# Kernel tuning notes

Hardware: AMD Instinct MI355X
Metric: run time of the kernel (lower is better)

The kernel has to match this reference:

```python
import jax, jax.numpy as jnp
import numpy as np

B, S, F, H = 256, 512, 64, 128
ODE_STEPS = 4
MAX_DT = 1.0


def setup_inputs() -> dict:
    key = jax.random.key(0)
    ks = jax.random.split(key, 11)
    D = F + H  # concat(x_t, h) width
    xav = float(np.sqrt(6.0 / (D + H)))          # xavier_uniform for gate weights
    bsc = float(1.0 / np.sqrt(D))                # torch Linear default bias init
    x = jax.random.normal(ks[0], (B, S, F), jnp.float32)
    time_diffs = jax.random.uniform(ks[1], (B, S), jnp.float32, 0.1, 2.0)
    def w(k):
        return jax.random.uniform(k, (D, H), jnp.float32, -xav, xav)
    def b(k):
        return jax.random.uniform(k, (H,), jnp.float32, -bsc, bsc)
    return {
        "x": x, "time_diffs": time_diffs,
        "W_i": w(ks[2]), "b_i": b(ks[3]),
        "W_f": w(ks[4]), "b_f": b(ks[5]),
        "W_o": w(ks[6]), "b_o": b(ks[7]),
        "W_g": w(ks[8]), "b_g": b(ks[9]),
    }


def reference(x, time_diffs, W_i, b_i, W_f, b_f, W_o, b_o, W_g, b_g):
    def ode_func(x_t, h, c):
        comb = jnp.concatenate([x_t, h], axis=-1)  # [B, F+H]
        i = jax.nn.sigmoid(comb @ W_i + b_i)
        f = jax.nn.sigmoid(comb @ W_f + b_f)
        o = jax.nn.sigmoid(comb @ W_o + b_o)
        g = jnp.tanh(comb @ W_g + b_g)
        dc = i * g + f * c - c
        dh = o * jnp.tanh(c) - h
        return dh, dc

    def rk4_step(x_t, h, c, dt):  # dt: [B, 1]
        k1h, k1c = ode_func(x_t, h, c)
        k2h, k2c = ode_func(x_t, h + 0.5 * dt * k1h, c + 0.5 * dt * k1c)
        k3h, k3c = ode_func(x_t, h + 0.5 * dt * k2h, c + 0.5 * dt * k2c)
        k4h, k4c = ode_func(x_t, h + dt * k3h, c + dt * k3c)
        h_new = h + dt / 6.0 * (k1h + 2 * k2h + 2 * k3h + k4h)
        c_new = c + dt / 6.0 * (k1c + 2 * k2c + 2 * k3c + k4c)
        return h_new, c_new

    def time_step(carry, inp):
        h, c = carry
        x_t, dtv = inp  # x_t [B,F], dtv [B]
        sub_dt = (jnp.minimum(dtv, MAX_DT) / ODE_STEPS)[:, None]  # [B,1]
        def body(hc, _):
            hh, cc = hc
            return rk4_step(x_t, hh, cc, sub_dt), None
        (h, c), _ = jax.lax.scan(body, (h, c), None, length=ODE_STEPS)
        return (h, c), h

    h0 = jnp.zeros((x.shape[0], H), x.dtype)
    c0 = jnp.zeros((x.shape[0], H), x.dtype)
    xs = (jnp.swapaxes(x, 0, 1), jnp.swapaxes(time_diffs, 0, 1))  # [S,B,F], [S,B]
    _, hs = jax.lax.scan(time_step, (h0, c0), xs)  # [S,B,H]
    return jnp.swapaxes(hs, 0, 1)  # [B,S,H]
```

## Files before the change

kernel.cpp:

```cpp
#include <hip/hip_runtime.h>


#define B_N 256
#define S_N 512
#define F_N 64
#define H_N 128

typedef _Float16 v8h __attribute__((ext_vector_type(8)));
typedef float v4f __attribute__((ext_vector_type(4)));

#define PIN_V(x) asm("" : "+v"(x))
#define MFMA16(a, b, c) __builtin_amdgcn_mfma_f32_16x16x32_f16((a), (b), (c), 0, 0, 0)
#define SB0() __builtin_amdgcn_sched_barrier(0)
#define BAR() do { SB0(); \
                   asm volatile("s_waitcnt lgkmcnt(0)" ::: "memory"); \
                   __builtin_amdgcn_s_barrier(); SB0(); } while (0)

static __device__ __forceinline__ float sigm(float x) {
  float e = __builtin_amdgcn_exp2f(-1.442695040888963f * x);
  return __builtin_amdgcn_rcpf(1.0f + e);
}

__global__ void __launch_bounds__(512, 2) clstm_mfma10(
    const float* __restrict__ x,
    const float* __restrict__ td,
    const float* __restrict__ Wi, const float* __restrict__ bi,
    const float* __restrict__ Wf, const float* __restrict__ bff,
    const float* __restrict__ Wo, const float* __restrict__ bo,
    const float* __restrict__ Wg, const float* __restrict__ bg,
    float* __restrict__ out)
{
  const int b    = blockIdx.x;
  const int t    = threadIdx.x;
  const int wv   = t >> 6;
  const int l    = t & 63;
  const int col  = l & 15;
  const int quad = l >> 4;
  const int n    = wv * 16 + col;

  const float* Wptr[4] = {Wi, Wf, Wo, Wg};

  v8h Bh[4][4];
  v8h Bx[4][2];
#pragma unroll
  for (int g = 0; g < 4; ++g) {
    const float* W = Wptr[g];
#pragma unroll
    for (int kt = 0; kt < 4; ++kt) {
      v8h f;
#pragma unroll
      for (int j = 0; j < 8; ++j)
        f[j] = (_Float16)W[(64 + kt * 32 + quad * 8 + j) * H_N + n];
      Bh[g][kt] = f;
      PIN_V(Bh[g][kt]);
    }
#pragma unroll
    for (int kt = 0; kt < 2; ++kt) {
      v8h f;
#pragma unroll
      for (int j = 0; j < 8; ++j)
        f[j] = (_Float16)W[(kt * 32 + quad * 8 + j) * H_N + n];
      Bx[g][kt] = f;
      PIN_V(Bx[g][kt]);
    }
  }
  float bias[4];
#pragma unroll
  for (int g = 0; g < 4; ++g)
    bias[g] = (g == 0 ? bi : g == 1 ? bff : g == 2 ? bo : bg)[n];

  __shared__ alignas(16) _Float16 lds_h[2][H_N];
  __shared__ alignas(16) _Float16 lds_x[F_N];
  __shared__ float lds_td[S_N];

  lds_td[t] = td[b * S_N + t];
  if (t < 32) {
    const float* xr = x + (size_t)b * S_N * F_N;
    lds_x[2 * t]     = (_Float16)xr[2 * t];
    lds_x[2 * t + 1] = (_Float16)xr[2 * t + 1];
  }
  if (t < H_N) lds_h[0][t] = (_Float16)0.0f;

  float h0v = 0.f, c0v = 0.f;
  float h_ev = 0.f, c_ev = 0.f;
  float sum_h = 0.f, sum_c = 0.f;
  float dt = 0.f, hdt = 0.f, d6 = 0.f, d6p = 0.f;
  const v4f zf = {0.f, 0.f, 0.f, 0.f};
  v4f ci2 = zf, ci3 = zf, cf2 = zf, cf3 = zf, cg2 = zf, cg3 = zf;
  v4f xpI = zf, xpF = zf, xpO = zf, xpG = zf;
  float xn0 = 0.f, xn1 = 0.f;

  for (int s = 0; s < S_N; ++s) {
#pragma unroll
    for (int ode = 0; ode < 4; ++ode) {
#pragma unroll
      for (int st = 0; st < 4; ++st) {
        BAR();
        const _Float16* hb = lds_h[st & 1];
        v8h ah0 = *(const v8h*)(hb + quad * 8);
        v8h ah1 = *(const v8h*)(hb + 32 + quad * 8);
        v8h ah2 = *(const v8h*)(hb + 64 + quad * 8);
        v8h ah3 = *(const v8h*)(hb + 96 + quad * 8);

        if (ode == 0 && st == 0) {
          dt  = fminf(lds_td[s], 1.0f) * 0.25f;
          hdt = 0.5f * dt;
          d6  = dt * (1.0f / 6.0f);
          v8h ax0 = *(const v8h*)(lds_x + quad * 8);
          v8h ax1 = *(const v8h*)(lds_x + 32 + quad * 8);
          {
            v4f cb = {bias[0], bias[0], bias[0], bias[0]};
            v4f a = MFMA16(ax0, Bx[0][0], cb);  xpI = MFMA16(ax1, Bx[0][1], a);
          }
          {
            v4f cb = {bias[1], bias[1], bias[1], bias[1]};
            v4f a = MFMA16(ax0, Bx[1][0], cb);  xpF = MFMA16(ax1, Bx[1][1], a);
          }
          {
            v4f cb = {bias[2], bias[2], bias[2], bias[2]};
            v4f a = MFMA16(ax0, Bx[2][0], cb);  xpO = MFMA16(ax1, Bx[2][1], a);
          }
          {
            v4f cb = {bias[3], bias[3], bias[3], bias[3]};
            v4f a = MFMA16(ax0, Bx[3][0], cb);  xpG = MFMA16(ax1, Bx[3][1], a);
          }
          xn0 = 0.f; xn1 = 0.f;
          if (t < 32 && s + 1 < S_N) {
            const float* xr = x + (size_t)(b * S_N + s + 1) * F_N;
            xn0 = xr[2 * t]; xn1 = xr[2 * t + 1];
          }
        }

        v4f co0 = MFMA16(ah0, Bh[2][0], xpO);
        v4f co1 = MFMA16(ah1, Bh[2][1], zf);
        v4f co2 = MFMA16(ah2, Bh[2][2], zf);
        v4f co3 = MFMA16(ah3, Bh[2][3], zf);
        SB0();

        float tc;
        {
          const int pr = (st == 0) ? 3 : st - 1;
          float pi = ci2[0] + ci3[0];
          float pf = cf2[0] + cf3[0];
          float pg = cg2[0] + cg3[0];
          float ai = sigm(pi);
          float af = sigm(pf);
          float ag = fmaf(2.0f, sigm(2.0f * pg), -1.0f);
          float kc = fmaf(ai, ag, (af - 1.0f) * c_ev);
          float cnx;
          if (pr == 0)      { sum_c = kc;                      cnx = fmaf(hdt, kc, c0v); }
          else if (pr == 1) { sum_c = fmaf(2.f, kc, sum_c);    cnx = fmaf(hdt, kc, c0v); }
          else if (pr == 2) { sum_c = fmaf(2.f, kc, sum_c);    cnx = fmaf(dt, kc, c0v); }
          else {
            float sc = sum_c + kc;
            float dd = (ode == 0 && st == 0) ? d6p : d6;
            c0v = fmaf(dd, sc, c0v);
            cnx = c0v;
          }
          c_ev = cnx;
          tc = fmaf(2.0f, sigm(2.0f * c_ev), -1.0f);
        }

        float po = (co0[0] + co1[0]) + (co2[0] + co3[0]);
        float ao = sigm(po);
        float kh = fmaf(ao, tc, -h_ev);
        float hnx;
        if (st == 0)      { sum_h = kh;                      hnx = fmaf(hdt, kh, h0v); }
        else if (st == 1) { sum_h = fmaf(2.f, kh, sum_h);    hnx = fmaf(hdt, kh, h0v); }
        else if (st == 2) { sum_h = fmaf(2.f, kh, sum_h);    hnx = fmaf(dt, kh, h0v); }
        else {
          float sh = sum_h + kh;
          h0v = fmaf(d6, sh, h0v);
          hnx = h0v;
        }
        h_ev = hnx;
        if (quad == 0) lds_h[(st & 1) ^ 1][n] = (_Float16)hnx;
        SB0();

        ci2 = MFMA16(ah0, Bh[0][0], xpI);
        ci2 = MFMA16(ah1, Bh[0][1], ci2);
        ci3 = MFMA16(ah2, Bh[0][2], zf);
        ci3 = MFMA16(ah3, Bh[0][3], ci3);
        cf2 = MFMA16(ah0, Bh[1][0], xpF);
        cf2 = MFMA16(ah1, Bh[1][1], cf2);
        cf3 = MFMA16(ah2, Bh[1][2], zf);
        cf3 = MFMA16(ah3, Bh[1][3], cf3);
        cg2 = MFMA16(ah0, Bh[3][0], xpG);
        cg2 = MFMA16(ah1, Bh[3][1], cg2);
        cg3 = MFMA16(ah2, Bh[3][2], zf);
        cg3 = MFMA16(ah3, Bh[3][3], cg3);
        SB0();

        if (ode == 3 && st == 3) {
          if (t < 32 && s + 1 < S_N) {
            lds_x[2 * t]     = (_Float16)xn0;
            lds_x[2 * t + 1] = (_Float16)xn1;
          }
          if (quad == 0) out[(size_t)(b * S_N + s) * H_N + n] = h0v;
          d6p = d6;
        }
      }
    }
  }
}

extern "C" void kernel_launch(void* const* d_in, const int* in_sizes, int n_in,
                              void* d_out, int out_size, void* d_ws, size_t ws_size,
                              hipStream_t stream) {
  (void)in_sizes; (void)n_in; (void)d_ws; (void)ws_size; (void)out_size;
  clstm_mfma10<<<B_N, 512, 0, stream>>>(
      (const float*)d_in[0],
      (const float*)d_in[1],
      (const float*)d_in[2], (const float*)d_in[3],
      (const float*)d_in[4], (const float*)d_in[5],
      (const float*)d_in[6], (const float*)d_in[7],
      (const float*)d_in[8], (const float*)d_in[9],
      (float*)d_out);
}
```

Measured before the change: 3.406 ms.

## Stagger IFG MFMA and gate-activation order across wave parities

Splits waves into two parity groups. One group runs the i/f/g-gate activation math before issuing the i/f/g MFMA block, the other issues the MFMAs first. The IFG MFMAs now come before the h update and LDS store instead of after. The goal is for waves sharing a SIMD to interleave matrix-core work with transcendental VALU work, so the two units overlap rather than contend. This adds divergent code paths by wave, plus register pinning that could raise register pressure.

Measured after the change: 3.952 ms. 1.16x slower.

```diff
diff --git a/kernel.cpp b/kernel.cpp
--- a/kernel.cpp
+++ b/kernel.cpp
@@ -16,12 +16,40 @@
                    asm volatile("s_waitcnt lgkmcnt(0)" ::: "memory"); \
                    __builtin_amdgcn_s_barrier(); SB0(); } while (0)
 
+#define IFG_BLOCK() do { \
+  ci2 = MFMA16(ah0, Bh[0][0], xpI); ci2 = MFMA16(ah1, Bh[0][1], ci2); \
+  ci3 = MFMA16(ah2, Bh[0][2], zf);  ci3 = MFMA16(ah3, Bh[0][3], ci3); \
+  cf2 = MFMA16(ah0, Bh[1][0], xpF); cf2 = MFMA16(ah1, Bh[1][1], cf2); \
+  cf3 = MFMA16(ah2, Bh[1][2], zf);  cf3 = MFMA16(ah3, Bh[1][3], cf3); \
+  cg2 = MFMA16(ah0, Bh[3][0], xpG); cg2 = MFMA16(ah1, Bh[3][1], cg2); \
+  cg3 = MFMA16(ah2, Bh[3][2], zf);  cg3 = MFMA16(ah3, Bh[3][3], cg3); \
+} while (0)
+
+#define S1_BLOCK(PR, CROSS) do { \
+  float ai = sigm(pi); \
+  float af = sigm(pf); \
+  float ag = fmaf(2.0f, sigm(2.0f * pg), -1.0f); \
+  float kc = fmaf(ai, ag, (af - 1.0f) * c_ev); \
+  float cnx; \
+  if ((PR) == 0)      { sum_c = kc;                   cnx = fmaf(hdt, kc, c0v); } \
+  else if ((PR) == 1) { sum_c = fmaf(2.f, kc, sum_c); cnx = fmaf(hdt, kc, c0v); } \
+  else if ((PR) == 2) { sum_c = fmaf(2.f, kc, sum_c); cnx = fmaf(dt, kc, c0v); } \
+  else { \
+    float sc = sum_c + kc; \
+    float dd = (CROSS) ? d6p : d6; \
+    c0v = fmaf(dd, sc, c0v); \
+    cnx = c0v; \
+  } \
+  c_ev = cnx; \
+  tc = fmaf(2.0f, sigm(2.0f * c_ev), -1.0f); \
+} while (0)
+
 static __device__ __forceinline__ float sigm(float x) {
   float e = __builtin_amdgcn_exp2f(-1.442695040888963f * x);
   return __builtin_amdgcn_rcpf(1.0f + e);
 }
 
-__global__ void __launch_bounds__(512, 2) clstm_mfma10(
+__global__ void __launch_bounds__(512, 2) clstm_mfma11(
     const float* __restrict__ x,
     const float* __restrict__ td,
     const float* __restrict__ Wi, const float* __restrict__ bi,
@@ -37,6 +65,7 @@
   const int col  = l & 15;
   const int quad = l >> 4;
   const int n    = wv * 16 + col;
+  const int par  = (wv ^ (wv >> 2)) & 1;
 
   const float* Wptr[4] = {Wi, Wf, Wo, Wg};
 
@@ -135,31 +164,29 @@
         v4f co1 = MFMA16(ah1, Bh[2][1], zf);
         v4f co2 = MFMA16(ah2, Bh[2][2], zf);
         v4f co3 = MFMA16(ah3, Bh[2][3], zf);
+
+        float pi = ci2[0] + ci3[0];
+        float pf = cf2[0] + cf3[0];
+        float pg = cg2[0] + cg3[0];
+        const int pr = (st == 0) ? 3 : st - 1;
+        const bool cross = (ode == 0 && st == 0);
+        float tc;
         SB0();
 
-        float tc;
-        {
-          const int pr = (st == 0) ? 3 : st - 1;
-          float pi = ci2[0] + ci3[0];
-          float pf = cf2[0] + cf3[0];
-          float pg = cg2[0] + cg3[0];
-          float ai = sigm(pi);
-          float af = sigm(pf);
-          float ag = fmaf(2.0f, sigm(2.0f * pg), -1.0f);
-          float kc = fmaf(ai, ag, (af - 1.0f) * c_ev);
-          float cnx;
-          if (pr == 0)      { sum_c = kc;                      cnx = fmaf(hdt, kc, c0v); }
-          else if (pr == 1) { sum_c = fmaf(2.f, kc, sum_c);    cnx = fmaf(hdt, kc, c0v); }
-          else if (pr == 2) { sum_c = fmaf(2.f, kc, sum_c);    cnx = fmaf(dt, kc, c0v); }
-          else {
-            float sc = sum_c + kc;
-            float dd = (ode == 0 && st == 0) ? d6p : d6;
-            c0v = fmaf(dd, sc, c0v);
-            cnx = c0v;
-          }
-          c_ev = cnx;
-          tc = fmaf(2.0f, sigm(2.0f * c_ev), -1.0f);
-        }
+        if (par) {
+          PIN_V(pi); PIN_V(pf); PIN_V(pg);
+          S1_BLOCK(pr, cross);
+          SB0();
+          PIN_V(ah0); PIN_V(ah1); PIN_V(ah2); PIN_V(ah3);
+          IFG_BLOCK();
+        } else {
+          PIN_V(ah0); PIN_V(ah1); PIN_V(ah2); PIN_V(ah3);
+          IFG_BLOCK();
+          SB0();
+          PIN_V(pi); PIN_V(pf); PIN_V(pg);
+          S1_BLOCK(pr, cross);
+        }
+        SB0();
 
         float po = (co0[0] + co1[0]) + (co2[0] + co3[0]);
         float ao = sigm(po);
@@ -175,21 +202,6 @@
         }
         h_ev = hnx;
         if (quad == 0) lds_h[(st & 1) ^ 1][n] = (_Float16)hnx;
-        SB0();
-
-        ci2 = MFMA16(ah0, Bh[0][0], xpI);
-        ci2 = MFMA16(ah1, Bh[0][1], ci2);
-        ci3 = MFMA16(ah2, Bh[0][2], zf);
-        ci3 = MFMA16(ah3, Bh[0][3], ci3);
-        cf2 = MFMA16(ah0, Bh[1][0], xpF);
-        cf2 = MFMA16(ah1, Bh[1][1], cf2);
-        cf3 = MFMA16(ah2, Bh[1][2], zf);
-        cf3 = MFMA16(ah3, Bh[1][3], cf3);
-        cg2 = MFMA16(ah0, Bh[3][0], xpG);
-        cg2 = MFMA16(ah1, Bh[3][1], cg2);
-        cg3 = MFMA16(ah2, Bh[3][2], zf);
-        cg3 = MFMA16(ah3, Bh[3][3], cg3);
-        SB0();
 
         if (ode == 3 && st == 3) {
           if (t < 32 && s + 1 < S_N) {
@@ -208,7 +220,7 @@
                               void* d_out, int out_size, void* d_ws, size_t ws_size,
                               hipStream_t stream) {
   (void)in_sizes; (void)n_in; (void)d_ws; (void)ws_size; (void)out_size;
-  clstm_mfma10<<<B_N, 512, 0, stream>>>(
+  clstm_mfma11<<<B_N, 512, 0, stream>>>(
       (const float*)d_in[0],
       (const float*)d_in[1],
       (const float*)d_in[2], (const float*)d_in[3],
```

## Specialize waves into gate-preactivation producers and output/state-update consumers via LDS

Applied to the files above, without the earlier changes.

Splits the eight waves into two roles. Four waves compute the i/f/g gate preactivations for 32 columns each and publish them to a double-buffered LDS array. The other four compute the o-gate, read the i/f/g values one stage later and perform the cell and hidden state updates. This replaces uniform per-wave work, where each wave ran all four gates and the full update serially, with a split that overlaps the gate MFMAs and the update math across waves. In exchange it adds LDS traffic and more registers per wave, since each wave now holds weights for two column tiles, and it leaves the two roles with unequal work.

Measured after the change: 4.773 ms. +40.1%, slower.

```diff
diff --git a/kernel.cpp b/kernel.cpp
--- a/kernel.cpp
+++ b/kernel.cpp
@@ -9,7 +9,6 @@
 typedef _Float16 v8h __attribute__((ext_vector_type(8)));
 typedef float v4f __attribute__((ext_vector_type(4)));
 
-#define PIN_V(x) asm("" : "+v"(x))
 #define MFMA16(a, b, c) __builtin_amdgcn_mfma_f32_16x16x32_f16((a), (b), (c), 0, 0, 0)
 #define SB0() __builtin_amdgcn_sched_barrier(0)
 #define BAR() do { SB0(); \
@@ -21,7 +20,37 @@
   return __builtin_amdgcn_rcpf(1.0f + e);
 }
 
-__global__ void __launch_bounds__(512, 2) clstm_mfma10(
+#define UPD(SUF) do { \
+  float ai = sigm(pi_##SUF); \
+  float af = sigm(pf_##SUF); \
+  float ag = fmaf(2.0f, sigm(2.0f * pg_##SUF), -1.0f);        \
+  float kc = fmaf(ai, ag, (af - 1.0f) * c_ev_##SUF);          \
+  float cnx; \
+  if (pr == 0)      { sum_c_##SUF = kc;                         cnx = fmaf(hdt, kc, c0v_##SUF); } \
+  else if (pr == 1) { sum_c_##SUF = fmaf(2.f, kc, sum_c_##SUF); cnx = fmaf(hdt, kc, c0v_##SUF); } \
+  else if (pr == 2) { sum_c_##SUF = fmaf(2.f, kc, sum_c_##SUF); cnx = fmaf(dt, kc, c0v_##SUF); } \
+  else { \
+    float sc = sum_c_##SUF + kc; \
+    float dd = cross ? d6p : d6;                               \
+    c0v_##SUF = fmaf(dd, sc, c0v_##SUF); \
+    cnx = c0v_##SUF; \
+  } \
+  c_ev_##SUF = cnx; \
+  float tc = fmaf(2.0f, sigm(2.0f * c_ev_##SUF), -1.0f);      \
+  float ao = sigm(co_##SUF[0]); \
+  float kh = fmaf(ao, tc, -h_ev_##SUF);                       \
+  if (st == 0)      { sum_h_##SUF = kh;                         hnx_##SUF = fmaf(hdt, kh, h0v_##SUF); } \
+  else if (st == 1) { sum_h_##SUF = fmaf(2.f, kh, sum_h_##SUF); hnx_##SUF = fmaf(hdt, kh, h0v_##SUF); } \
+  else if (st == 2) { sum_h_##SUF = fmaf(2.f, kh, sum_h_##SUF); hnx_##SUF = fmaf(dt, kh, h0v_##SUF); } \
+  else { \
+    float sh = sum_h_##SUF + kh; \
+    h0v_##SUF = fmaf(d6, sh, h0v_##SUF); \
+    hnx_##SUF = h0v_##SUF; \
+  } \
+  h_ev_##SUF = hnx_##SUF; \
+} while (0)
+
+__global__ void __launch_bounds__(512, 2) clstm_mfma12(
     const float* __restrict__ x,
     const float* __restrict__ td,
     const float* __restrict__ Wi, const float* __restrict__ bi,
@@ -34,46 +63,74 @@
   const int t    = threadIdx.x;
   const int wv   = t >> 6;
   const int l    = t & 63;
-  const int col  = l & 15;
   const int quad = l >> 4;
-  const int n    = wv * 16 + col;
-
-  const float* Wptr[4] = {Wi, Wf, Wo, Wg};
-
-  v8h Bh[4][4];
-  v8h Bx[4][2];
-#pragma unroll
-  for (int g = 0; g < 4; ++g) {
-    const float* W = Wptr[g];
-#pragma unroll
-    for (int kt = 0; kt < 4; ++kt) {
-      v8h f;
-#pragma unroll
-      for (int j = 0; j < 8; ++j)
-        f[j] = (_Float16)W[(64 + kt * 32 + quad * 8 + j) * H_N + n];
-      Bh[g][kt] = f;
-      PIN_V(Bh[g][kt]);
+  const int role = (wv ^ (wv >> 2)) & 1;
+  const int sl   = ((wv >> 1) & 1) + 2 * ((wv >> 2) & 1);
+  const int n0   = sl * 32 + (l & 15);
+
+  __shared__ alignas(16) _Float16 lds_h[2][H_N];
+  __shared__ alignas(16) _Float16 lds_x[F_N];
+  __shared__ float lds_p[2][3][H_N];
+  __shared__ float lds_td[S_N];
+
+  v8h BhA[3][2][4]; v8h BxA[3][2][2]; float biA[3][2];
+  v8h BhO[2][4];    v8h BxO[2][2];    float biO[2];
+
+  if (role == 0) {
+    const float* Wg3[3] = {Wi, Wf, Wg};
+    const float* bg3[3] = {bi, bff, bg};
+#pragma unroll
+    for (int g = 0; g < 3; ++g) {
+#pragma unroll
+      for (int T = 0; T < 2; ++T) {
+        const float* W = Wg3[g];
+        const int nc = n0 + T * 16;
+#pragma unroll
+        for (int kt = 0; kt < 4; ++kt) {
+          v8h f;
+#pragma unroll
+          for (int j = 0; j < 8; ++j)
+            f[j] = (_Float16)W[(64 + kt * 32 + quad * 8 + j) * H_N + nc];
+          BhA[g][T][kt] = f;
+        }
+#pragma unroll
+        for (int kx = 0; kx < 2; ++kx) {
+          v8h f;
+#pragma unroll
+          for (int j = 0; j < 8; ++j)
+            f[j] = (_Float16)W[(kx * 32 + quad * 8 + j) * H_N + nc];
+          BxA[g][T][kx] = f;
+        }
+        biA[g][T] = bg3[g][nc];
+      }
     }
-#pragma unroll
-    for (int kt = 0; kt < 2; ++kt) {
-      v8h f;
-#pragma unroll
-      for (int j = 0; j < 8; ++j)
-        f[j] = (_Float16)W[(kt * 32 + quad * 8 + j) * H_N + n];
-      Bx[g][kt] = f;
-      PIN_V(Bx[g][kt]);
+  } else {
+#pragma unroll
+    for (int T = 0; T < 2; ++T) {
+      const int nc = n0 + T * 16;
+#pragma unroll
+      for (int kt = 0; kt < 4; ++kt) {
+        v8h f;
+#pragma unroll
+        for (int j = 0; j < 8; ++j)
+          f[j] = (_Float16)Wo[(64 + kt * 32 + quad * 8 + j) * H_N + nc];
+        BhO[T][kt] = f;
+      }
+#pragma unroll
+      for (int kx = 0; kx < 2; ++kx) {
+        v8h f;
+#pragma unroll
+        for (int j = 0; j < 8; ++j)
+          f[j] = (_Float16)Wo[(kx * 32 + quad * 8 + j) * H_N + nc];
+        BxO[T][kx] = f;
+      }
+      biO[T] = bo[nc];
     }
   }
-  float bias[4];
-#pragma unroll
-  for (int g = 0; g < 4; ++g)
-    bias[g] = (g == 0 ? bi : g == 1 ? bff : g == 2 ? bo : bg)[n];
-
-  __shared__ alignas(16) _Float16 lds_h[2][H_N];
-  __shared__ alignas(16) _Float16 lds_x[F_N];
-  __shared__ float lds_td[S_N];
 
   lds_td[t] = td[b * S_N + t];
+  ((float*)lds_p)[t] = 0.f;
+  if (t < 256) ((float*)lds_p)[512 + t] = 0.f;
   if (t < 32) {
     const float* xr = x + (size_t)b * S_N * F_N;
     lds_x[2 * t]     = (_Float16)xr[2 * t];
@@ -81,13 +138,12 @@
   }
   if (t < H_N) lds_h[0][t] = (_Float16)0.0f;
 
-  float h0v = 0.f, c0v = 0.f;
-  float h_ev = 0.f, c_ev = 0.f;
-  float sum_h = 0.f, sum_c = 0.f;
+  const v4f zf = {0.f, 0.f, 0.f, 0.f};
+  float h0v_0 = 0.f, c0v_0 = 0.f, h_ev_0 = 0.f, c_ev_0 = 0.f, sum_h_0 = 0.f, sum_c_0 = 0.f;
+  float h0v_1 = 0.f, c0v_1 = 0.f, h_ev_1 = 0.f, c_ev_1 = 0.f, sum_h_1 = 0.f, sum_c_1 = 0.f;
   float dt = 0.f, hdt = 0.f, d6 = 0.f, d6p = 0.f;
-  const v4f zf = {0.f, 0.f, 0.f, 0.f};
-  v4f ci2 = zf, ci3 = zf, cf2 = zf, cf3 = zf, cg2 = zf, cg3 = zf;
-  v4f xpI = zf, xpF = zf, xpO = zf, xpG = zf;
+  v4f xpI_0 = zf, xpI_1 = zf, xpF_0 = zf, xpF_1 = zf, xpG_0 = zf, xpG_1 = zf;
+  v4f xpO_0 = zf, xpO_1 = zf;
   float xn0 = 0.f, xn1 = 0.f;
 
   for (int s = 0; s < S_N; ++s) {
@@ -102,102 +158,135 @@
         v8h ah2 = *(const v8h*)(hb + 64 + quad * 8);
         v8h ah3 = *(const v8h*)(hb + 96 + quad * 8);
 
-        if (ode == 0 && st == 0) {
-          dt  = fminf(lds_td[s], 1.0f) * 0.25f;
-          hdt = 0.5f * dt;
-          d6  = dt * (1.0f / 6.0f);
-          v8h ax0 = *(const v8h*)(lds_x + quad * 8);
-          v8h ax1 = *(const v8h*)(lds_x + 32 + quad * 8);
-          {
-            v4f cb = {bias[0], bias[0], bias[0], bias[0]};
-            v4f a = MFMA16(ax0, Bx[0][0], cb);  xpI = MFMA16(ax1, Bx[0][1], a);
-          }
-          {
-            v4f cb = {bias[1], bias[1], bias[1], bias[1]};
-            v4f a = MFMA16(ax0, Bx[1][0], cb);  xpF = MFMA16(ax1, Bx[1][1], a);
-          }
-          {
-            v4f cb = {bias[2], bias[2], bias[2], bias[2]};
-            v4f a = MFMA16(ax0, Bx[2][0], cb);  xpO = MFMA16(ax1, Bx[2][1], a);
-          }
-          {
-            v4f cb = {bias[3], bias[3], bias[3], bias[3]};
-            v4f a = MFMA16(ax0, Bx[3][0], cb);  xpG = MFMA16(ax1, Bx[3][1], a);
-          }
-          xn0 = 0.f; xn1 = 0.f;
-          if (t < 32 && s + 1 < S_N) {
-            const float* xr = x + (size_t)(b * S_N + s + 1) * F_N;
-            xn0 = xr[2 * t]; xn1 = xr[2 * t + 1];
-          }
-        }
-
-        v4f co0 = MFMA16(ah0, Bh[2][0], xpO);
-        v4f co1 = MFMA16(ah1, Bh[2][1], zf);
-        v4f co2 = MFMA16(ah2, Bh[2][2], zf);
-        v4f co3 = MFMA16(ah3, Bh[2][3], zf);
-        SB0();
-
-        float tc;
-        {
-          const int pr = (st == 0) ? 3 : st - 1;
-          float pi = ci2[0] + ci3[0];
-          float pf = cf2[0] + cf3[0];
-          float pg = cg2[0] + cg3[0];
-          float ai = sigm(pi);
-          float af = sigm(pf);
-          float ag = fmaf(2.0f, sigm(2.0f * pg), -1.0f);
-          float kc = fmaf(ai, ag, (af - 1.0f) * c_ev);
-          float cnx;
-          if (pr == 0)      { sum_c = kc;                      cnx = fmaf(hdt, kc, c0v); }
-          else if (pr == 1) { sum_c = fmaf(2.f, kc, sum_c);    cnx = fmaf(hdt, kc, c0v); }
-          else if (pr == 2) { sum_c = fmaf(2.f, kc, sum_c);    cnx = fmaf(dt, kc, c0v); }
-          else {
-            float sc = sum_c + kc;
-            float dd = (ode == 0 && st == 0) ? d6p : d6;
-            c0v = fmaf(dd, sc, c0v);
-            cnx = c0v;
-          }
-          c_ev = cnx;
-          tc = fmaf(2.0f, sigm(2.0f * c_ev), -1.0f);
-        }
-
-        float po = (co0[0] + co1[0]) + (co2[0] + co3[0]);
-        float ao = sigm(po);
-        float kh = fmaf(ao, tc, -h_ev);
-        float hnx;
-        if (st == 0)      { sum_h = kh;                      hnx = fmaf(hdt, kh, h0v); }
-        else if (st == 1) { sum_h = fmaf(2.f, kh, sum_h);    hnx = fmaf(hdt, kh, h0v); }
-        else if (st == 2) { sum_h = fmaf(2.f, kh, sum_h);    hnx = fmaf(dt, kh, h0v); }
-        else {
-          float sh = sum_h + kh;
-          h0v = fmaf(d6, sh, h0v);
-          hnx = h0v;
-        }
-        h_ev = hnx;
-        if (quad == 0) lds_h[(st & 1) ^ 1][n] = (_Float16)hnx;
-        SB0();
-
-        ci2 = MFMA16(ah0, Bh[0][0], xpI);
-        ci2 = MFMA16(ah1, Bh[0][1], ci2);
-        ci3 = MFMA16(ah2, Bh[0][2], zf);
-        ci3 = MFMA16(ah3, Bh[0][3], ci3);
-        cf2 = MFMA16(ah0, Bh[1][0], xpF);
-        cf2 = MFMA16(ah1, Bh[1][1], cf2);
-        cf3 = MFMA16(ah2, Bh[1][2], zf);
-        cf3 = MFMA16(ah3, Bh[1][3], cf3);
-        cg2 = MFMA16(ah0, Bh[3][0], xpG);
-        cg2 = MFMA16(ah1, Bh[3][1], cg2);
-        cg3 = MFMA16(ah2, Bh[3][2], zf);
-        cg3 = MFMA16(ah3, Bh[3][3], cg3);
-        SB0();
-
-        if (ode == 3 && st == 3) {
-          if (t < 32 && s + 1 < S_N) {
+        if (role == 0) {
+          if (ode == 0 && st == 0) {
+            v8h ax0 = *(const v8h*)(lds_x + quad * 8);
+            v8h ax1 = *(const v8h*)(lds_x + 32 + quad * 8);
+            {
+              v4f cb = {biA[0][0], biA[0][0], biA[0][0], biA[0][0]};
+              v4f u = MFMA16(ax0, BxA[0][0][0], cb);
+              xpI_0 = MFMA16(ax1, BxA[0][0][1], u);
+            }
+            {
+              v4f cb = {biA[0][1], biA[0][1], biA[0][1], biA[0][1]};
+              v4f u = MFMA16(ax0, BxA[0][1][0], cb);
+              xpI_1 = MFMA16(ax1, BxA[0][1][1], u);
+            }
+            {
+              v4f cb = {biA[1][0], biA[1][0], biA[1][0], biA[1][0]};
+              v4f u = MFMA16(ax0, BxA[1][0][0], cb);
+              xpF_0 = MFMA16(ax1, BxA[1][0][1], u);
+            }
+            {
+              v4f cb = {biA[1][1], biA[1][1], biA[1][1], biA[1][1]};
+              v4f u = MFMA16(ax0, BxA[1][1][0], cb);
+              xpF_1 = MFMA16(ax1, BxA[1][1][1], u);
+            }
+            {
+              v4f cb = {biA[2][0], biA[2][0], biA[2][0], biA[2][0]};
+              v4f u = MFMA16(ax0, BxA[2][0][0], cb);
+              xpG_0 = MFMA16(ax1, BxA[2][0][1], u);
+            }
+            {
+              v4f cb = {biA[2][1], biA[2][1], biA[2][1], biA[2][1]};
+              v4f u = MFMA16(ax0, BxA[2][1][0], cb);
+              xpG_1 = MFMA16(ax1, BxA[2][1][1], u);
+            }
+            xn0 = 0.f; xn1 = 0.f;
+            if (t < 32 && s + 1 < S_N) {
+              const float* xr = x + (size_t)(b * S_N + s + 1) * F_N;
+              xn0 = xr[2 * t]; xn1 = xr[2 * t + 1];
+            }
+          }
+
+          v4f aI0 = MFMA16(ah0, BhA[0][0][0], xpI_0);
+          v4f aF0 = MFMA16(ah0, BhA[1][0][0], xpF_0);
+          v4f aG0 = MFMA16(ah0, BhA[2][0][0], xpG_0);
+          v4f aI1 = MFMA16(ah0, BhA[0][1][0], xpI_1);
+          v4f aF1 = MFMA16(ah0, BhA[1][1][0], xpF_1);
+          v4f aG1 = MFMA16(ah0, BhA[2][1][0], xpG_1);
+          aI0 = MFMA16(ah1, BhA[0][0][1], aI0);
+          aF0 = MFMA16(ah1, BhA[1][0][1], aF0);
+          aG0 = MFMA16(ah1, BhA[2][0][1], aG0);
+          aI1 = MFMA16(ah1, BhA[0][1][1], aI1);
+          aF1 = MFMA16(ah1, BhA[1][1][1], aF1);
+          aG1 = MFMA16(ah1, BhA[2][1][1], aG1);
+          aI0 = MFMA16(ah2, BhA[0][0][2], aI0);
+          aF0 = MFMA16(ah2, BhA[1][0][2], aF0);
+          aG0 = MFMA16(ah2, BhA[2][0][2], aG0);
+          aI1 = MFMA16(ah2, BhA[0][1][2], aI1);
+          aF1 = MFMA16(ah2, BhA[1][1][2], aF1);
+          aG1 = MFMA16(ah2, BhA[2][1][2], aG1);
+          aI0 = MFMA16(ah3, BhA[0][0][3], aI0);
+          aF0 = MFMA16(ah3, BhA[1][0][3], aF0);
+          aG0 = MFMA16(ah3, BhA[2][0][3], aG0);
+          aI1 = MFMA16(ah3, BhA[0][1][3], aI1);
+          aF1 = MFMA16(ah3, BhA[1][1][3], aF1);
+          aG1 = MFMA16(ah3, BhA[2][1][3], aG1);
+
+          float v0 = (quad == 0) ? aI0[0] : (quad == 1) ? aF0[0] : aG0[0];
+          float v1 = (quad == 0) ? aI1[0] : (quad == 1) ? aF1[0] : aG1[0];
+          if (quad < 3) {
+            float* pb = &lds_p[(st & 1) ^ 1][quad][0];
+            pb[n0]      = v0;
+            pb[n0 + 16] = v1;
+          }
+
+          if (ode == 3 && st == 3 && t < 32 && s + 1 < S_N) {
             lds_x[2 * t]     = (_Float16)xn0;
             lds_x[2 * t + 1] = (_Float16)xn1;
           }
-          if (quad == 0) out[(size_t)(b * S_N + s) * H_N + n] = h0v;
-          d6p = d6;
+        } else {
+          if (ode == 0 && st == 0) {
+            dt  = fminf(lds_td[s], 1.0f) * 0.25f;
+            hdt = 0.5f * dt;
+            d6  = dt * (1.0f / 6.0f);
+            v8h ax0 = *(const v8h*)(lds_x + quad * 8);
+            v8h ax1 = *(const v8h*)(lds_x + 32 + quad * 8);
+            {
+              v4f cb = {biO[0], biO[0], biO[0], biO[0]};
+              v4f u = MFMA16(ax0, BxO[0][0], cb);
+              xpO_0 = MFMA16(ax1, BxO[0][1], u);
+            }
+            {
+              v4f cb = {biO[1], biO[1], biO[1], biO[1]};
+              v4f u = MFMA16(ax0, BxO[1][0], cb);
+              xpO_1 = MFMA16(ax1, BxO[1][1], u);
+            }
+          }
+
+          const float* pb = &lds_p[st & 1][0][0];
+          float pi_0 = pb[n0],             pi_1 = pb[n0 + 16];
+          float pf_0 = pb[H_N + n0],       pf_1 = pb[H_N + n0 + 16];
+          float pg_0 = pb[2 * H_N + n0],   pg_1 = pb[2 * H_N + n0 + 16];
+
+          v4f co_0 = MFMA16(ah0, BhO[0][0], xpO_0);
+          v4f co_1 = MFMA16(ah0, BhO[1][0], xpO_1);
+          co_0 = MFMA16(ah1, BhO[0][1], co_0);
+          co_1 = MFMA16(ah1, BhO[1][1], co_1);
+          co_0 = MFMA16(ah2, BhO[0][2], co_0);
+          co_1 = MFMA16(ah2, BhO[1][2], co_1);
+          co_0 = MFMA16(ah3, BhO[0][3], co_0);
+          co_1 = MFMA16(ah3, BhO[1][3], co_1);
+
+          const int pr = (st == 0) ? 3 : st - 1;
+          const bool cross = (ode == 0 && st == 0);
+          float hnx_0, hnx_1;
+          UPD(0);
+          UPD(1);
+
+          if (quad == 0) {
+            lds_h[(st & 1) ^ 1][n0]      = (_Float16)hnx_0;
+            lds_h[(st & 1) ^ 1][n0 + 16] = (_Float16)hnx_1;
+          }
+
+          if (ode == 3 && st == 3) {
+            if (quad == 0) {
+              out[(size_t)(b * S_N + s) * H_N + n0]      = h0v_0;
+              out[(size_t)(b * S_N + s) * H_N + n0 + 16] = h0v_1;
+            }
+            d6p = d6;
+          }
         }
       }
     }
@@ -208,7 +297,7 @@
                               void* d_out, int out_size, void* d_ws, size_t ws_size,
                               hipStream_t stream) {
   (void)in_sizes; (void)n_in; (void)d_ws; (void)ws_size; (void)out_size;
-  clstm_mfma10<<<B_N, 512, 0, stream>>>(
+  clstm_mfma12<<<B_N, 512, 0, stream>>>(
       (const float*)d_in[0],
       (const float*)d_in[1],
       (const float*)d_in[2], (const float*)d_in[3],
```
